# Kernel optimization log

Hardware: AMD Instinct MI355X
Metric: run time of the kernel (lower is better)

Reference implementation:

```python
import jax, jax.numpy as jnp
import numpy as np


def bilinear_sampler(img, flow):
    """Warp img (B,H,W,C) by per-pixel flow (B,H,W,2): sample at (x+u, y+v).
    Border handling: indices clipped to the image (edge padding)."""
    B, H, W, C = img.shape
    gy, gx = jnp.meshgrid(jnp.arange(H, dtype=img.dtype),
                          jnp.arange(W, dtype=img.dtype), indexing='ij')
    x = gx[None] + flow[..., 0]  # (B,H,W)
    y = gy[None] + flow[..., 1]
    x0f = jnp.floor(x)
    y0f = jnp.floor(y)
    wx = x - x0f  # fractional parts, differentiable w.r.t. flow
    wy = y - y0f
    x0 = jnp.clip(x0f.astype(jnp.int32), 0, W - 1)
    x1 = jnp.clip(x0f.astype(jnp.int32) + 1, 0, W - 1)
    y0 = jnp.clip(y0f.astype(jnp.int32), 0, H - 1)
    y1 = jnp.clip(y0f.astype(jnp.int32) + 1, 0, H - 1)
    b = jnp.arange(B)[:, None, None]
    Ia = img[b, y0, x0]  # (B,H,W,C)
    Ib = img[b, y1, x0]
    Ic = img[b, y0, x1]
    Id = img[b, y1, x1]
    wx = wx[..., None]
    wy = wy[..., None]
    return (Ia * (1 - wx) * (1 - wy) + Ib * (1 - wx) * wy
            + Ic * wx * (1 - wy) + Id * wx * wy)


def setup_inputs() -> dict:
    key = jax.random.key(0)
    k1, k2, k3, k4, k5, k6 = jax.random.split(key, 6)
    B, H, W = 8, 512, 512
    return {
        't': jax.random.uniform(k1, (B, 1, 1, 1), dtype=jnp.float32),
        'I0': jax.random.uniform(k2, (B, H, W, 3), dtype=jnp.float32),
        'I1': jax.random.uniform(k3, (B, H, W, 3), dtype=jnp.float32),
        'interp': jax.random.normal(k4, (B, H, W, 5), dtype=jnp.float32),
        'Fhat_t0': jax.random.normal(k5, (B, H, W, 2), dtype=jnp.float32),
        'Fhat_t1': jax.random.normal(k6, (B, H, W, 2), dtype=jnp.float32),
    }


def reference(t, I0, I1, interp, Fhat_t0, Fhat_t1):
    Ft0 = interp[..., 0:2] + Fhat_t0
    Ft1 = interp[..., 2:4] + Fhat_t1
    Vt0 = jax.nn.sigmoid(interp[..., 4:5])  # (B,H,W,1) -> broadcasts over RGB
    Vt1 = 1.0 - Vt0
    g0 = bilinear_sampler(I0, Ft0)
    g1 = bilinear_sampler(I1, Ft1)
    eps = 1e-12
    w0 = (1.0 - t) * Vt0
    w1 = t * Vt1
    It = (w0 * g0 + w1 * g1) / (w0 + w1 + eps)
    return It
```

## Files before the change

kernel.cpp:

```cpp
#include <hip/hip_runtime.h>
#include <hip/hip_fp16.h>

constexpr int B_ = 8;
constexpr int H_ = 512;
constexpr int W_ = 512;
constexpr int HW_ = H_ * W_;

constexpr int TS = 32;
constexpr int R_ = 4;
constexpr int RS = TS + 2 * R_;
constexpr int NSPX = RS * RS;


template <int IMG>
__device__ __forceinline__ void sampleT(const __half2* __restrict__ rgp,
                                        const __half2* __restrict__ bbp,
                                        const float* __restrict__ img,
                                        int gx0, int gy0,
                                        float sx, float sy, float g[3]) {
    float xf = floorf(sx), yf = floorf(sy);
    float wx = sx - xf, wy = sy - yf;
    int ix = (int)xf, iy = (int)yf;
    int x0 = min(max(ix, 0), W_ - 1);
    int x1 = min(max(ix + 1, 0), W_ - 1);
    int y0 = min(max(iy, 0), H_ - 1);
    int y1 = min(max(iy + 1, 0), H_ - 1);

    float w00 = (1.0f - wx) * (1.0f - wy);
    float w01 = wx * (1.0f - wy);
    float w10 = (1.0f - wx) * wy;
    float w11 = wx * wy;

    int lx0 = x0 - gx0, lx1 = x1 - gx0;
    int ly0 = y0 - gy0, ly1 = y1 - gy0;
    bool inT = ((unsigned)lx0 < (unsigned)RS) & ((unsigned)lx1 < (unsigned)RS) &
               ((unsigned)ly0 < (unsigned)RS) & ((unsigned)ly1 < (unsigned)RS);

    if (inT) {
        int p00 = ly0 * RS + lx0, p01 = ly0 * RS + lx1;
        int p10 = ly1 * RS + lx0, p11 = ly1 * RS + lx1;
        __half2 h00 = __float2half2_rn(w00);
        __half2 h01 = __float2half2_rn(w01);
        __half2 h10 = __float2half2_rn(w10);
        __half2 h11 = __float2half2_rn(w11);
        __half2 rg = __hmul2(h00, rgp[p00]);
        rg = __hfma2(h01, rgp[p01], rg);
        rg = __hfma2(h10, rgp[p10], rg);
        rg = __hfma2(h11, rgp[p11], rg);
        __half2 bb = __hmul2(h00, bbp[p00]);
        bb = __hfma2(h01, bbp[p01], bb);
        bb = __hfma2(h10, bbp[p10], bb);
        bb = __hfma2(h11, bbp[p11], bb);
        g[0] = __low2float(rg);
        g[1] = __high2float(rg);
        g[2] = (IMG == 0) ? __low2float(bb) : __high2float(bb);
    } else {
        const float* pa = img + ((size_t)y0 * W_ + x0) * 3;
        const float* pb = img + ((size_t)y0 * W_ + x1) * 3;
        const float* pc = img + ((size_t)y1 * W_ + x0) * 3;
        const float* pd = img + ((size_t)y1 * W_ + x1) * 3;
        #pragma unroll
        for (int ch = 0; ch < 3; ++ch)
            g[ch] = pa[ch] * w00 + pb[ch] * w01 +
                    pc[ch] * w10 + pd[ch] * w11;
    }
}

__global__ __launch_bounds__(256, 4) void frame_interp_tiled(
    const float* __restrict__ t,
    const float* __restrict__ I0,
    const float* __restrict__ I1,
    const float* __restrict__ interp,
    const float* __restrict__ F0,
    const float* __restrict__ F1,
    float* __restrict__ out)
{
    __shared__ __half2 lds_rg[2][NSPX];
    __shared__ __half2 lds_bb[NSPX];

    int tid = threadIdx.x;
    int bid = blockIdx.x;
    int b    = bid & 7;
    int tile = bid >> 3;
    int ty   = tile >> 4;
    int tx   = tile & 15;
    int gx0 = tx * TS - R_;
    int gy0 = ty * TS - R_;

    const float* img0 = I0 + (size_t)b * HW_ * 3;
    const float* img1 = I1 + (size_t)b * HW_ * 3;

    float tb = t[b];

    constexpr int FULL = NSPX / 256;
    constexpr int TAIL = NSPX - FULL * 256;
    float c0[FULL][3], c1[FULL][3];
    #pragma unroll
    for (int k = 0; k < FULL; ++k) {
        int p = tid + k * 256;
        int ry = p / RS;
        int rx = p - ry * RS;
        int gy = min(max(gy0 + ry, 0), H_ - 1);
        int gx = min(max(gx0 + rx, 0), W_ - 1);
        size_t s = ((size_t)gy * W_ + gx) * 3;
        __builtin_memcpy(c0[k], img0 + s, 12);
        __builtin_memcpy(c1[k], img1 + s, 12);
    }
    float d0[3], d1[3];
    bool tail = tid < TAIL;
    int pt = FULL * 256 + tid;
    if (tail) {
        int ry = pt / RS;
        int rx = pt - ry * RS;
        int gy = min(max(gy0 + ry, 0), H_ - 1);
        int gx = min(max(gx0 + rx, 0), W_ - 1);
        size_t s = ((size_t)gy * W_ + gx) * 3;
        __builtin_memcpy(d0, img0 + s, 12);
        __builtin_memcpy(d1, img1 + s, 12);
    }

    int row  = tid >> 3;
    int colb = (tid & 7) * 4;
    int gy_o = ty * TS + row;
    int gx_o = tx * TS + colb;
    size_t idx0 = (size_t)b * HW_ + (size_t)gy_o * W_ + gx_o;

    const float* ipp = (const float*)__builtin_assume_aligned(interp + idx0 * 5, 16);
    const float* f0p = (const float*)__builtin_assume_aligned(F0 + idx0 * 2, 16);
    const float* f1p = (const float*)__builtin_assume_aligned(F1 + idx0 * 2, 16);
    float ii[20], f0v[8], f1v[8];
    __builtin_memcpy(ii, ipp, 80);
    __builtin_memcpy(f0v, f0p, 32);
    __builtin_memcpy(f1v, f1p, 32);

    __builtin_amdgcn_sched_barrier(0);

    #pragma unroll
    for (int k = 0; k < FULL; ++k) {
        int p = tid + k * 256;
        lds_rg[0][p] = __floats2half2_rn(c0[k][0], c0[k][1]);
        lds_rg[1][p] = __floats2half2_rn(c1[k][0], c1[k][1]);
        lds_bb[p]    = __floats2half2_rn(c0[k][2], c1[k][2]);
    }
    if (tail) {
        lds_rg[0][pt] = __floats2half2_rn(d0[0], d0[1]);
        lds_rg[1][pt] = __floats2half2_rn(d1[0], d1[1]);
        lds_bb[pt]    = __floats2half2_rn(d0[2], d1[2]);
    }
    __syncthreads();

    float o[12];
    #pragma unroll
    for (int k = 0; k < 4; ++k) {
        float fx = (float)(gx_o + k);
        float fy = (float)gy_o;
        float sx0 = fx + ii[k * 5 + 0] + f0v[k * 2 + 0];
        float sy0 = fy + ii[k * 5 + 1] + f0v[k * 2 + 1];
        float sx1 = fx + ii[k * 5 + 2] + f1v[k * 2 + 0];
        float sy1 = fy + ii[k * 5 + 3] + f1v[k * 2 + 1];
        float vt0 = 1.0f / (1.0f + __expf(-ii[k * 5 + 4]));

        float g0[3], g1[3];
        sampleT<0>(lds_rg[0], lds_bb, img0, gx0, gy0, sx0, sy0, g0);
        sampleT<1>(lds_rg[1], lds_bb, img1, gx0, gy0, sx1, sy1, g1);

        float w0 = (1.0f - tb) * vt0;
        float w1 = tb * (1.0f - vt0);
        float inv = 1.0f / (w0 + w1 + 1e-12f);
        o[k * 3 + 0] = (w0 * g0[0] + w1 * g1[0]) * inv;
        o[k * 3 + 1] = (w0 * g0[1] + w1 * g1[1]) * inv;
        o[k * 3 + 2] = (w0 * g0[2] + w1 * g1[2]) * inv;
    }
    float* op = (float*)__builtin_assume_aligned(out + idx0 * 3, 16);
    __builtin_memcpy(op, o, 48);
}

extern "C" void kernel_launch(void* const* d_in, const int* in_sizes, int n_in,
                              void* d_out, int out_size, void* d_ws, size_t ws_size,
                              hipStream_t stream) {
    const float* t      = (const float*)d_in[0];
    const float* I0     = (const float*)d_in[1];
    const float* I1     = (const float*)d_in[2];
    const float* interp = (const float*)d_in[3];
    const float* F0     = (const float*)d_in[4];
    const float* F1     = (const float*)d_in[5];
    float* out = (float*)d_out;

    int blocks = B_ * (H_ / TS) * (W_ / TS);
    frame_interp_tiled<<<blocks, 256, 0, stream>>>(t, I0, I1, interp, F0, F1, out);
}
```

Baseline: 164.7 us.

## Process four tiles per block with double-buffered LDS and prefetch

Each block now handles four horizontally adjacent tiles instead of one. The LDS staging buffers are double-buffered, and global loads for the next tile's image halo and flow streams are issued before the current tile is computed, so load latency overlaps with sampling. This cuts the block count by four and lowers the launch-bounds occupancy hint from 4 to 2 blocks per CU, which adds register and LDS pressure and reduces parallelism across CUs.

```diff
diff --git a/kernel.cpp b/kernel.cpp
--- a/kernel.cpp
+++ b/kernel.cpp
@@ -10,6 +10,9 @@
 constexpr int R_ = 4;
 constexpr int RS = TS + 2 * R_;
 constexpr int NSPX = RS * RS;
+constexpr int NT = 4;
+constexpr int FULL = NSPX / 256;
+constexpr int TAIL = NSPX - FULL * 256;
 
 
 template <int IMG>
@@ -66,7 +69,39 @@
     }
 }
 
-__global__ __launch_bounds__(256, 4) void frame_interp_tiled(
+#define LOAD_STAGE(TX) do {                                                  \
+    int _gx0 = (TX) * TS - R_;                                               \
+    _Pragma("unroll")                                                        \
+    for (int k = 0; k < FULL; ++k) {                                         \
+        int p = tid + k * 256;                                               \
+        int ry = p / RS;                                                     \
+        int rx = p - ry * RS;                                                \
+        int gy = min(max(gy0 + ry, 0), H_ - 1);                              \
+        int gx = min(max(_gx0 + rx, 0), W_ - 1);                             \
+        size_t s = ((size_t)gy * W_ + gx) * 3;                               \
+        __builtin_memcpy(c0[k], img0 + s, 12);                               \
+        __builtin_memcpy(c1[k], img1 + s, 12);                               \
+    }                                                                        \
+    if (tid < TAIL) {                                                        \
+        int p = FULL * 256 + tid;                                            \
+        int ry = p / RS;                                                     \
+        int rx = p - ry * RS;                                                \
+        int gy = min(max(gy0 + ry, 0), H_ - 1);                              \
+        int gx = min(max(_gx0 + rx, 0), W_ - 1);                             \
+        size_t s = ((size_t)gy * W_ + gx) * 3;                               \
+        __builtin_memcpy(d0, img0 + s, 12);                                  \
+        __builtin_memcpy(d1, img1 + s, 12);                                  \
+    }                                                                        \
+} while (0)
+
+#define LOAD_STREAMS(TX, PAR) do {                                           \
+    size_t _idx = (size_t)b * HW_ + (size_t)gy_o * W_ + ((TX) * TS + colb);  \
+    __builtin_memcpy(ii[(PAR)], interp + _idx * 5, 80);                      \
+    __builtin_memcpy(f0v[(PAR)], F0 + _idx * 2, 32);                         \
+    __builtin_memcpy(f1v[(PAR)], F1 + _idx * 2, 32);                         \
+} while (0)
+
+__global__ __launch_bounds__(256, 2) void frame_interp_pers(
     const float* __restrict__ t,
     const float* __restrict__ I0,
     const float* __restrict__ I1,
@@ -75,104 +110,87 @@
     const float* __restrict__ F1,
     float* __restrict__ out)
 {
-    __shared__ __half2 lds_rg[2][NSPX];
-    __shared__ __half2 lds_bb[NSPX];
+    __shared__ __half2 lds_rg[2][2][NSPX];
+    __shared__ __half2 lds_bb[2][NSPX];
 
     int tid = threadIdx.x;
     int bid = blockIdx.x;
-    int b    = bid & 7;
-    int tile = bid >> 3;
-    int ty   = tile >> 4;
-    int tx   = tile & 15;
-    int gx0 = tx * TS - R_;
+    int b  = bid & 7;
+    int w  = bid >> 3;
+    int ty = w >> 2;
+    int txb = (w & 3) * 4;
+
     int gy0 = ty * TS - R_;
-
     const float* img0 = I0 + (size_t)b * HW_ * 3;
     const float* img1 = I1 + (size_t)b * HW_ * 3;
-
     float tb = t[b];
-
-    constexpr int FULL = NSPX / 256;
-    constexpr int TAIL = NSPX - FULL * 256;
-    float c0[FULL][3], c1[FULL][3];
-    #pragma unroll
-    for (int k = 0; k < FULL; ++k) {
-        int p = tid + k * 256;
-        int ry = p / RS;
-        int rx = p - ry * RS;
-        int gy = min(max(gy0 + ry, 0), H_ - 1);
-        int gx = min(max(gx0 + rx, 0), W_ - 1);
-        size_t s = ((size_t)gy * W_ + gx) * 3;
-        __builtin_memcpy(c0[k], img0 + s, 12);
-        __builtin_memcpy(c1[k], img1 + s, 12);
-    }
-    float d0[3], d1[3];
-    bool tail = tid < TAIL;
-    int pt = FULL * 256 + tid;
-    if (tail) {
-        int ry = pt / RS;
-        int rx = pt - ry * RS;
-        int gy = min(max(gy0 + ry, 0), H_ - 1);
-        int gx = min(max(gx0 + rx, 0), W_ - 1);
-        size_t s = ((size_t)gy * W_ + gx) * 3;
-        __builtin_memcpy(d0, img0 + s, 12);
-        __builtin_memcpy(d1, img1 + s, 12);
-    }
 
     int row  = tid >> 3;
     int colb = (tid & 7) * 4;
     int gy_o = ty * TS + row;
-    int gx_o = tx * TS + colb;
-    size_t idx0 = (size_t)b * HW_ + (size_t)gy_o * W_ + gx_o;
-
-    const float* ipp = (const float*)__builtin_assume_aligned(interp + idx0 * 5, 16);
-    const float* f0p = (const float*)__builtin_assume_aligned(F0 + idx0 * 2, 16);
-    const float* f1p = (const float*)__builtin_assume_aligned(F1 + idx0 * 2, 16);
-    float ii[20], f0v[8], f1v[8];
-    __builtin_memcpy(ii, ipp, 80);
-    __builtin_memcpy(f0v, f0p, 32);
-    __builtin_memcpy(f1v, f1p, 32);
-
-    __builtin_amdgcn_sched_barrier(0);
+
+    float c0[FULL][3], c1[FULL][3], d0[3], d1[3];
+    float ii[2][20], f0v[2][8], f1v[2][8];
+
+    LOAD_STAGE(txb);
+    LOAD_STREAMS(txb, 0);
 
     #pragma unroll
-    for (int k = 0; k < FULL; ++k) {
-        int p = tid + k * 256;
-        lds_rg[0][p] = __floats2half2_rn(c0[k][0], c0[k][1]);
-        lds_rg[1][p] = __floats2half2_rn(c1[k][0], c1[k][1]);
-        lds_bb[p]    = __floats2half2_rn(c0[k][2], c1[k][2]);
+    for (int i = 0; i < NT; ++i) {
+        int tx  = txb + i;
+        int gx0 = tx * TS - R_;
+        int buf = i & 1;
+
+        #pragma unroll
+        for (int k = 0; k < FULL; ++k) {
+            int p = tid + k * 256;
+            lds_rg[buf][0][p] = __floats2half2_rn(c0[k][0], c0[k][1]);
+            lds_rg[buf][1][p] = __floats2half2_rn(c1[k][0], c1[k][1]);
+            lds_bb[buf][p]    = __floats2half2_rn(c0[k][2], c1[k][2]);
+        }
+        if (tid < TAIL) {
+            int p = FULL * 256 + tid;
+            lds_rg[buf][0][p] = __floats2half2_rn(d0[0], d0[1]);
+            lds_rg[buf][1][p] = __floats2half2_rn(d1[0], d1[1]);
+            lds_bb[buf][p]    = __floats2half2_rn(d0[2], d1[2]);
+        }
+
+        if (i + 1 < NT) {
+            LOAD_STAGE(txb + i + 1);
+            LOAD_STREAMS(txb + i + 1, (i + 1) & 1);
+        }
+        __builtin_amdgcn_sched_barrier(0);
+
+        asm volatile("s_waitcnt lgkmcnt(0)" ::: "memory");
+        __builtin_amdgcn_s_barrier();
+        __builtin_amdgcn_sched_barrier(0);
+
+        int gx_o = tx * TS + colb;
+        size_t idx0 = (size_t)b * HW_ + (size_t)gy_o * W_ + gx_o;
+        float o[12];
+        #pragma unroll
+        for (int k = 0; k < 4; ++k) {
+            float fx = (float)(gx_o + k);
+            float fy = (float)gy_o;
+            float sx0 = fx + ii[buf][k * 5 + 0] + f0v[buf][k * 2 + 0];
+            float sy0 = fy + ii[buf][k * 5 + 1] + f0v[buf][k * 2 + 1];
+            float sx1 = fx + ii[buf][k * 5 + 2] + f1v[buf][k * 2 + 0];
+            float sy1 = fy + ii[buf][k * 5 + 3] + f1v[buf][k * 2 + 1];
+            float vt0 = 1.0f / (1.0f + __expf(-ii[buf][k * 5 + 4]));
+
+            float g0[3], g1[3];
+            sampleT<0>(lds_rg[buf][0], lds_bb[buf], img0, gx0, gy0, sx0, sy0, g0);
+            sampleT<1>(lds_rg[buf][1], lds_bb[buf], img1, gx0, gy0, sx1, sy1, g1);
+
+            float w0 = (1.0f - tb) * vt0;
+            float w1 = tb * (1.0f - vt0);
+            float inv = 1.0f / (w0 + w1 + 1e-12f);
+            o[k * 3 + 0] = (w0 * g0[0] + w1 * g1[0]) * inv;
+            o[k * 3 + 1] = (w0 * g0[1] + w1 * g1[1]) * inv;
+            o[k * 3 + 2] = (w0 * g0[2] + w1 * g1[2]) * inv;
+        }
+        __builtin_memcpy(out + idx0 * 3, o, 48);
     }
-    if (tail) {
-        lds_rg[0][pt] = __floats2half2_rn(d0[0], d0[1]);
-        lds_rg[1][pt] = __floats2half2_rn(d1[0], d1[1]);
-        lds_bb[pt]    = __floats2half2_rn(d0[2], d1[2]);
-    }
-    __syncthreads();
-
-    float o[12];
-    #pragma unroll
-    for (int k = 0; k < 4; ++k) {
-        float fx = (float)(gx_o + k);
-        float fy = (float)gy_o;
-        float sx0 = fx + ii[k * 5 + 0] + f0v[k * 2 + 0];
-        float sy0 = fy + ii[k * 5 + 1] + f0v[k * 2 + 1];
-        float sx1 = fx + ii[k * 5 + 2] + f1v[k * 2 + 0];
-        float sy1 = fy + ii[k * 5 + 3] + f1v[k * 2 + 1];
-        float vt0 = 1.0f / (1.0f + __expf(-ii[k * 5 + 4]));
-
-        float g0[3], g1[3];
-        sampleT<0>(lds_rg[0], lds_bb, img0, gx0, gy0, sx0, sy0, g0);
-        sampleT<1>(lds_rg[1], lds_bb, img1, gx0, gy0, sx1, sy1, g1);
-
-        float w0 = (1.0f - tb) * vt0;
-        float w1 = tb * (1.0f - vt0);
-        float inv = 1.0f / (w0 + w1 + 1e-12f);
-        o[k * 3 + 0] = (w0 * g0[0] + w1 * g1[0]) * inv;
-        o[k * 3 + 1] = (w0 * g0[1] + w1 * g1[1]) * inv;
-        o[k * 3 + 2] = (w0 * g0[2] + w1 * g1[2]) * inv;
-    }
-    float* op = (float*)__builtin_assume_aligned(out + idx0 * 3, 16);
-    __builtin_memcpy(op, o, 48);
 }
 
 extern "C" void kernel_launch(void* const* d_in, const int* in_sizes, int n_in,
@@ -186,6 +204,6 @@
     const float* F1     = (const float*)d_in[5];
     float* out = (float*)d_out;
 
-    int blocks = B_ * (H_ / TS) * (W_ / TS);
-    frame_interp_tiled<<<blocks, 256, 0, stream>>>(t, I0, I1, interp, F0, F1, out);
+    int blocks = B_ * (H_ / TS) * (W_ / TS) / NT;
+    frame_interp_pers<<<blocks, 256, 0, stream>>>(t, I0, I1, interp, F0, F1, out);
 }
```

After: 165.7 us. No clear change (+0.6%).
